# Optimization experiments

Measured on AMD Instinct MI355X. Metric: run time of the kernel, lower is better.

The kernel has to match this reference:

```python
import jax, jax.numpy as jnp
import numpy as np

EPS = 1e-5
DIL = 2
PAD = 2  # dilation * (kernel_size - 1) // 2


def _conv(x, w, dil, pad):
    return jax.lax.conv_general_dilated(
        x, w, window_strides=(1, 1), padding=[(pad, pad), (pad, pad)],
        rhs_dilation=(dil, dil), dimension_numbers=('NCHW', 'OIHW', 'NCHW'))


def _bn(x, g, b):
    # BatchNorm2d in training mode: per-channel batch stats over (N,H,W)
    m = x.mean(axis=(0, 2, 3), keepdims=True)
    v = x.var(axis=(0, 2, 3), keepdims=True)
    return (x - m) * jax.lax.rsqrt(v + EPS) * g[None, :, None, None] + b[None, :, None, None]


def _deform_conv(x, offset, w, dil=DIL, pad=PAD):
    # torchvision deform_conv2d v1 (no modulation): offset [B, 2*K, H, W] with
    # channel ordering (dy_0, dx_0, dy_1, dx_1, ...), kernel tap k = ky*3 + kx.
    B, C, H, W = x.shape
    Co = w.shape[0]
    K = 9
    off = offset.reshape(B, K, 2, H, W)
    dy, dx = off[:, :, 0], off[:, :, 1]              # [B,K,H,W]
    kr = jnp.arange(3)
    kyy = (jnp.repeat(kr, 3) * dil - pad).astype(x.dtype)   # [K]
    kxx = (jnp.tile(kr, 3) * dil - pad).astype(x.dtype)     # [K]
    hg = jnp.arange(H, dtype=x.dtype)
    wg = jnp.arange(W, dtype=x.dtype)
    py = hg[None, None, :, None] + kyy[None, :, None, None] + dy   # [B,K,H,W]
    px = wg[None, None, None, :] + kxx[None, :, None, None] + dx   # [B,K,H,W]
    y0 = jnp.floor(py)
    x0 = jnp.floor(px)
    wy = py - y0   # [B,K,H,W]
    wx = px - x0
    y0i = y0.astype(jnp.int32)
    x0i = x0.astype(jnp.int32)
    x_flat = x.reshape(B, C, H * W)

    def corner(yi, xi):
        valid = ((yi >= 0) & (yi < H) & (xi >= 0) & (xi < W)).astype(x.dtype)  # [B,K,H,W]
        idx = jnp.clip(yi, 0, H - 1) * W + jnp.clip(xi, 0, W - 1)
        v = jax.vmap(lambda xb, ib: xb[:, ib])(x_flat, idx.reshape(B, -1))    # [B,C,K*H*W]
        return v.reshape(B, C, K, H, W) * valid[:, None]

    v00 = corner(y0i, x0i)
    v01 = corner(y0i, x0i + 1)
    v10 = corner(y0i + 1, x0i)
    v11 = corner(y0i + 1, x0i + 1)
    wy_ = wy[:, None]   # [B,1,K,H,W]
    wx_ = wx[:, None]
    sampled = (v00 * (1 - wy_) * (1 - wx_) + v01 * (1 - wy_) * wx_
               + v10 * wy_ * (1 - wx_) + v11 * wy_ * wx_)          # [B,C,K,H,W]
    return jnp.einsum('bckhw,ock->bohw', sampled, w.reshape(Co, C, K))


def setup_inputs() -> dict:
    key = jax.random.key(0)
    ks = jax.random.split(key, 4)
    B, C, H, W = 4, 256, 56, 56
    x = jax.random.normal(ks[0], (B, C, H, W), dtype=jnp.float32)
    w_off = jax.random.normal(ks[1], (18, C, 3, 3), dtype=jnp.float32) * 0.01
    b_off = jnp.zeros((18,), dtype=jnp.float32)
    w1 = jax.random.normal(ks[2], (C, C, 3, 3), dtype=jnp.float32) * (1.0 / np.sqrt(9 * C))
    w2 = jax.random.normal(ks[3], (C, C, 3, 3), dtype=jnp.float32) * (1.0 / np.sqrt(9 * C))
    gamma1 = jnp.ones((C,), dtype=jnp.float32)
    beta1 = jnp.zeros((C,), dtype=jnp.float32)
    gamma2 = jnp.ones((C,), dtype=jnp.float32)
    beta2 = jnp.zeros((C,), dtype=jnp.float32)
    return {'x': x, 'w_off': w_off, 'b_off': b_off, 'w1': w1, 'gamma1': gamma1,
            'beta1': beta1, 'w2': w2, 'gamma2': gamma2, 'beta2': beta2}


def reference(x, w_off, b_off, w1, gamma1, beta1, w2, gamma2, beta2):
    offset = _conv(x, w_off, DIL, PAD) + b_off[None, :, None, None]   # [B,18,H,W]
    out = _deform_conv(x, offset, w1)
    out = jax.nn.relu(_bn(out, gamma1, beta1))
    out = _conv(out, w2, 1, 1)
    out = _bn(out, gamma2, beta2)
    return jax.nn.relu(out + x)
```

## Files before the change

### kernel.cpp

```cpp
#include <hip/hip_runtime.h>

typedef __bf16 bf16;
typedef bf16 bf16x4 __attribute__((ext_vector_type(4)));
typedef bf16 bf16x8 __attribute__((ext_vector_type(8)));
typedef float f32x4 __attribute__((ext_vector_type(4)));

#define CH 256
#define HH 56
#define WW 56
#define HW 3136
#define MM 12544
#define KT 2304

__device__ __forceinline__ void gll16(const bf16* g, bf16* l) {
  __builtin_amdgcn_global_load_lds(
      (const __attribute__((address_space(1))) void*)g,
      (__attribute__((address_space(3))) void*)l, 16, 0, 0);
}

__global__ __launch_bounds__(256) void nchw2nhwc_k(const float* __restrict__ x,
                                                   bf16* __restrict__ o) {
  __shared__ float t[32][33];
  const int b = blockIdx.z, hw0 = blockIdx.x * 32, c0 = blockIdx.y * 32;
  const int tid = threadIdx.x;
  {
    const int cl = tid >> 3, hwl = (tid & 7) * 4;
    f32x4 v = *(const f32x4*)&x[(size_t)(b * CH + c0 + cl) * HW + hw0 + hwl];
#pragma unroll
    for (int i = 0; i < 4; ++i) t[cl][hwl + i] = v[i];
  }
  __syncthreads();
  const int hwl = tid >> 3, cl = (tid & 7) * 4;
  bf16x4 ov;
#pragma unroll
  for (int i = 0; i < 4; ++i) ov[i] = (bf16)t[cl + i][hwl];
  *(bf16x4*)&o[(size_t)(b * HW + hw0 + hwl) * CH + c0 + cl] = ov;
}

__global__ void reorder_w_k(const float* __restrict__ in, bf16* __restrict__ out,
                            int Nsrc, int Ntot) {
  const int idx = blockIdx.x * 256 + threadIdx.x;
  if (idx >= Ntot * KT) return;
  const int o = idx / KT, r = idx - o * KT;
  const int k = r >> 8, c = r & 255;
  float v = (o < Nsrc) ? in[(size_t)(o * CH + c) * 9 + k] : 0.f;
  out[idx] = (bf16)v;
}

__global__ __launch_bounds__(256) void build_deform_k(
    const bf16* __restrict__ xn, const float* __restrict__ offb,
    const float* __restrict__ boff, bf16* __restrict__ A1) {
  const int tid = threadIdx.x;
  const int m = blockIdx.x * 32 + (tid >> 3);
  const int l7 = tid & 7;
  const int b = m / HW, hw = m - b * HW;
  const int h = hw / WW, w = hw - h * WW;
  const float* orow = offb + m * 18;
  const bf16* xb = xn + (size_t)b * HW * CH;
  bf16* dst = A1 + (size_t)m * KT;
  for (int tap = 0; tap < 9; ++tap) {
    const int ky = tap / 3, kx = tap - ky * 3;
    const float dy = orow[2 * tap] + boff[2 * tap];
    const float dx = orow[2 * tap + 1] + boff[2 * tap + 1];
    const float py = (float)(h + ky * 2 - 2) + dy;
    const float px = (float)(w + kx * 2 - 2) + dx;
    const float y0f = floorf(py), x0f = floorf(px);
    const int y0 = (int)y0f, x0 = (int)x0f;
    const float wy = py - y0f, wx = px - x0f;
    const float w00 = (1.f - wy) * (1.f - wx), w01 = (1.f - wy) * wx;
    const float w10 = wy * (1.f - wx), w11 = wy * wx;
    const bool vy0 = (unsigned)y0 < HH, vy1 = (unsigned)(y0 + 1) < HH;
    const bool vx0 = (unsigned)x0 < WW, vx1 = (unsigned)(x0 + 1) < WW;
    const bf16* p00 = xb + (long long)(y0 * WW + x0) * CH;
#pragma unroll
    for (int j = 0; j < 4; ++j) {
      const int cc = j * 64 + l7 * 8;
      bf16x8 v00 = {}, v01 = {}, v10 = {}, v11 = {};
      if (vy0 && vx0) v00 = *(const bf16x8*)(p00 + cc);
      if (vy0 && vx1) v01 = *(const bf16x8*)(p00 + CH + cc);
      if (vy1 && vx0) v10 = *(const bf16x8*)(p00 + WW * CH + cc);
      if (vy1 && vx1) v11 = *(const bf16x8*)(p00 + WW * CH + CH + cc);
      bf16x8 o;
#pragma unroll
      for (int i = 0; i < 8; ++i)
        o[i] = (bf16)(w00 * (float)v00[i] + w01 * (float)v01[i] +
                      w10 * (float)v10[i] + w11 * (float)v11[i]);
      *(bf16x8*)(dst + tap * 256 + cc) = o;
    }
  }
}

template <int MODE, int EPI>
__global__ __launch_bounds__(256, 3) void gemm_k(
    const bf16* __restrict__ Asrc, const bf16* __restrict__ Bt,
    const bf16* __restrict__ zp, bf16* __restrict__ outb,
    float* __restrict__ sS, float* __restrict__ sQ,
    float* __restrict__ offout, const int ksteps, const int dil, const int pad) {
  __shared__ __align__(16) bf16 Ab[2][4096];
  __shared__ __align__(16) bf16 Bb[2][4096];
  const int tid = threadIdx.x;
  const int n0 = blockIdx.x * 64, m0 = blockIdx.y * 64;
  const int kbase = blockIdx.z * ksteps * 64;
  const int lane = tid & 63, wv = tid >> 6;
  const int wrM = wv >> 1, wcN = wv & 1;
  const int fr = lane & 15, kg = lane >> 4;
  const int srow = tid >> 3, cpos = tid & 7;
  const int sxor = (cpos ^ (srow & 7)) * 8;

  int bb[2], hh[2], wwv[2];
  const bf16* aptr[2];
  if (MODE == 1) {
#pragma unroll
    for (int pa = 0; pa < 2; ++pa) {
      const int m = m0 + pa * 32 + srow;
      bb[pa] = m / HW;
      const int hw = m - bb[pa] * HW;
      hh[pa] = hw / WW;
      wwv[pa] = hw - hh[pa] * WW;
    }
  } else {
#pragma unroll
    for (int pa = 0; pa < 2; ++pa)
      aptr[pa] = Asrc + (size_t)(m0 + pa * 32 + srow) * KT + kbase + sxor;
  }
  const bf16* bptr[2];
#pragma unroll
  for (int pb = 0; pb < 2; ++pb)
    bptr[pb] = Bt + (size_t)(n0 + pb * 32 + srow) * KT + kbase + sxor;

  f32x4 acc[2][2] = {};

  auto STAGE = [&](int kt, int buf) {
    const int kk = kbase + kt * 64;
#pragma unroll
    for (int pa = 0; pa < 2; ++pa) {
      const bf16* as;
      if (MODE == 0) {
        as = aptr[pa] + kt * 64;
      } else {
        const int tap = kk >> 8, coff = kk & 255;
        const int ky = tap / 3, kx = tap - ky * 3;
        const int y = hh[pa] + ky * dil - pad, xx = wwv[pa] + kx * dil - pad;
        const bool ok = ((unsigned)y < HH) && ((unsigned)xx < WW);
        as = ok ? Asrc + ((size_t)(bb[pa] * HW + y * WW + xx) * CH + coff + sxor)
                : zp + sxor;
      }
      gll16(as, &Ab[buf][(pa * 32 + srow) * 64 + cpos * 8]);
    }
#pragma unroll
    for (int pb = 0; pb < 2; ++pb)
      gll16(bptr[pb] + kt * 64, &Bb[buf][(pb * 32 + srow) * 64 + cpos * 8]);
  };

  auto COMPUTE = [&](int buf) {
#pragma unroll
    for (int kh = 0; kh < 2; ++kh) {
      bf16x8 af[2], bv[2];
#pragma unroll
      for (int mf = 0; mf < 2; ++mf) {
        const int row = wrM * 32 + mf * 16 + fr;
        const int g = (kh * 4 + kg) ^ (row & 7);
        af[mf] = *(const bf16x8*)&Ab[buf][row * 64 + g * 8];
      }
#pragma unroll
      for (int nf = 0; nf < 2; ++nf) {
        const int row = wcN * 32 + nf * 16 + fr;
        const int g = (kh * 4 + kg) ^ (row & 7);
        bv[nf] = *(const bf16x8*)&Bb[buf][row * 64 + g * 8];
      }
#pragma unroll
      for (int mf = 0; mf < 2; ++mf)
#pragma unroll
        for (int nf = 0; nf < 2; ++nf)
          acc[mf][nf] = __builtin_amdgcn_mfma_f32_16x16x32_bf16(af[mf], bv[nf],
                                                                acc[mf][nf], 0, 0, 0);
    }
  };

  STAGE(0, 0);
  __syncthreads();
  int buf = 0;
  for (int kt = 0; kt < ksteps; ++kt) {
    if (kt + 1 < ksteps) STAGE(kt + 1, buf ^ 1);
    COMPUTE(buf);
    __syncthreads();
    buf ^= 1;
  }

  if (EPI == 1) {
#pragma unroll
    for (int mf = 0; mf < 2; ++mf) {
      const int rr = m0 + wrM * 32 + mf * 16 + kg * 4;
#pragma unroll
      for (int nf = 0; nf < 2; ++nf) {
        const int col = n0 + wcN * 32 + nf * 16 + fr;
#pragma unroll
        for (int r = 0; r < 4; ++r)
          outb[(size_t)(rr + r) * CH + col] = (bf16)acc[mf][nf][r];
      }
    }
    float ps[2], pq[2];
#pragma unroll
    for (int nf = 0; nf < 2; ++nf) {
      float s = 0.f, q = 0.f;
#pragma unroll
      for (int mf = 0; mf < 2; ++mf)
#pragma unroll
        for (int r = 0; r < 4; ++r) {
          const float v = acc[mf][nf][r];
          s += v;
          q += v * v;
        }
      s += __shfl_xor(s, 16);
      s += __shfl_xor(s, 32);
      q += __shfl_xor(q, 16);
      q += __shfl_xor(q, 32);
      ps[nf] = s;
      pq[nf] = q;
    }
    float* red = (float*)&Ab[0][0];
    if (tid < 128) red[tid] = 0.f;
    __syncthreads();
    if (kg == 0) {
#pragma unroll
      for (int nf = 0; nf < 2; ++nf) {
        const int cb = wcN * 32 + nf * 16 + fr;
        atomicAdd(&red[cb], ps[nf]);
        atomicAdd(&red[64 + cb], pq[nf]);
      }
    }
    __syncthreads();
    if (tid < 64) {
      atomicAdd(&sS[n0 + tid], red[tid]);
      atomicAdd(&sQ[n0 + tid], red[64 + tid]);
    }
  } else {
#pragma unroll
    for (int mf = 0; mf < 2; ++mf) {
      const int rr = m0 + wrM * 32 + mf * 16 + kg * 4;
#pragma unroll
      for (int nf = 0; nf < 2; ++nf) {
        const int col = n0 + wcN * 32 + nf * 16 + fr;
        if (col < 18) {
#pragma unroll
          for (int r = 0; r < 4; ++r)
            atomicAdd(&offout[(size_t)(rr + r) * 18 + col], acc[mf][nf][r]);
        }
      }
    }
  }
}

__global__ void affine_k(const float* __restrict__ s, const float* __restrict__ sq,
                         const float* __restrict__ g, const float* __restrict__ be,
                         float* __restrict__ sc, float* __restrict__ bi) {
  const int c = threadIdx.x;
  const float inv = 1.f / (float)MM;
  const float mean = s[c] * inv;
  const float var = sq[c] * inv - mean * mean;
  const float scale = g[c] * rsqrtf(var + 1e-5f);
  sc[c] = scale;
  bi[c] = be[c] - mean * scale;
}

__global__ __launch_bounds__(256) void a1_kb(const bf16* __restrict__ in,
                                             const float* __restrict__ sc,
                                             const float* __restrict__ bi,
                                             bf16* __restrict__ out) {
  const size_t idx = (size_t)(blockIdx.x * 256 + threadIdx.x) * 8;
  const int c0 = (int)(idx & 255);
  bf16x8 v = *(const bf16x8*)&in[idx];
  bf16x8 o;
#pragma unroll
  for (int i = 0; i < 8; ++i) {
    float r = (float)v[i] * sc[c0 + i] + bi[c0 + i];
    o[i] = (bf16)(r > 0.f ? r : 0.f);
  }
  *(bf16x8*)&out[idx] = o;
}

__global__ __launch_bounds__(256) void final_kb(const bf16* __restrict__ o2,
                                                const float* __restrict__ x,
                                                const float* __restrict__ sc,
                                                const float* __restrict__ bi,
                                                float* __restrict__ out) {
  __shared__ float t[32][33];
  const int b = blockIdx.z, hw0 = blockIdx.x * 32, o0 = blockIdx.y * 32;
  const int tid = threadIdx.x;
  {
    const int hwl = tid >> 3, ol = (tid & 7) * 4;
    bf16x4 v = *(const bf16x4*)&o2[(size_t)(b * HW + hw0 + hwl) * CH + o0 + ol];
#pragma unroll
    for (int i = 0; i < 4; ++i) t[ol + i][hwl] = (float)v[i];
  }
  __syncthreads();
  const int ol = tid >> 3, hwl = (tid & 7) * 4;
  const int ch = o0 + ol;
  const float s = sc[ch], bb = bi[ch];
  const size_t xi = (size_t)(b * CH + ch) * HW + hw0 + hwl;
  f32x4 xv = *(const f32x4*)&x[xi];
  f32x4 r;
#pragma unroll
  for (int i = 0; i < 4; ++i) {
    float v = t[ol][hwl + i] * s + bb + xv[i];
    r[i] = v > 0.f ? v : 0.f;
  }
  *(f32x4*)&out[xi] = r;
}

#define WS_XN 0ULL
#define WS_W1T 6422528ULL
#define WS_W2T 7602176ULL
#define WS_WOF 8781824ULL
#define WS_OFFB 9076736ULL
#define WS_A1 9979904ULL
#define WS_O1 67782656ULL
#define WS_ACT 74205184ULL
#define WS_O2 80627712ULL
#define WS_ZP 87050240ULL
#define WS_STAT 87054336ULL
#define WS_SCB 87058432ULL

extern "C" void kernel_launch(void* const* d_in, const int* in_sizes, int n_in,
                              void* d_out, int out_size, void* d_ws, size_t ws_size,
                              hipStream_t stream) {
  const float* x = (const float*)d_in[0];
  const float* w_off = (const float*)d_in[1];
  const float* b_off = (const float*)d_in[2];
  const float* w1 = (const float*)d_in[3];
  const float* g1 = (const float*)d_in[4];
  const float* be1 = (const float*)d_in[5];
  const float* w2 = (const float*)d_in[6];
  const float* g2 = (const float*)d_in[7];
  const float* be2 = (const float*)d_in[8];
  float* out = (float*)d_out;
  char* ws = (char*)d_ws;

  bf16* xn = (bf16*)(ws + WS_XN);
  bf16* w1t = (bf16*)(ws + WS_W1T);
  bf16* w2t = (bf16*)(ws + WS_W2T);
  bf16* wof = (bf16*)(ws + WS_WOF);
  float* offb = (float*)(ws + WS_OFFB);
  bf16* A1 = (bf16*)(ws + WS_A1);
  bf16* o1 = (bf16*)(ws + WS_O1);
  bf16* act = (bf16*)(ws + WS_ACT);
  bf16* o2 = (bf16*)(ws + WS_O2);
  bf16* zp = (bf16*)(ws + WS_ZP);
  float* s1 = (float*)(ws + WS_STAT);
  float* sq1 = (float*)(ws + WS_STAT + 1024);
  float* s2 = (float*)(ws + WS_STAT + 2048);
  float* sq2 = (float*)(ws + WS_STAT + 3072);
  float* sc1 = (float*)(ws + WS_SCB);
  float* bi1 = (float*)(ws + WS_SCB + 1024);
  float* sc2 = (float*)(ws + WS_SCB + 2048);
  float* bi2 = (float*)(ws + WS_SCB + 3072);

  hipMemsetAsync(ws + WS_ZP, 0, 8192, stream);
  hipMemsetAsync(ws + WS_OFFB, 0, 903168, stream);

  nchw2nhwc_k<<<dim3(98, 8, 4), 256, 0, stream>>>(x, xn);
  reorder_w_k<<<2304, 256, 0, stream>>>(w1, w1t, 256, 256);
  reorder_w_k<<<2304, 256, 0, stream>>>(w2, w2t, 256, 256);
  reorder_w_k<<<576, 256, 0, stream>>>(w_off, wof, 18, 64);

  gemm_k<1, 0><<<dim3(1, 196, 4), 256, 0, stream>>>(xn, wof, zp, nullptr, nullptr,
                                                    nullptr, offb, 9, 2, 2);
  build_deform_k<<<392, 256, 0, stream>>>(xn, offb, b_off, A1);

  gemm_k<0, 1><<<dim3(4, 196, 1), 256, 0, stream>>>(A1, w1t, zp, o1, s1, sq1,
                                                    nullptr, 36, 0, 0);
  affine_k<<<1, 256, 0, stream>>>(s1, sq1, g1, be1, sc1, bi1);
  a1_kb<<<1568, 256, 0, stream>>>(o1, sc1, bi1, act);

  gemm_k<1, 1><<<dim3(4, 196, 1), 256, 0, stream>>>(act, w2t, zp, o2, s2, sq2,
                                                    nullptr, 36, 1, 1);
  affine_k<<<1, 256, 0, stream>>>(s2, sq2, g2, be2, sc2, bi2);

  final_kb<<<dim3(98, 8, 4), 256, 0, stream>>>(o2, x, sc2, bi2, out);
}
```

Before: 232.5 us.

## Use 128x128 split-K GEMM tiles with fp32 atomic output and separate stats pass

Replaces the 64x64 double-buffered GEMM for the two main convolutions with a 128x128 tile kernel that splits K three ways and accumulates into an fp32 buffer via atomicAdd. BN statistics move out of the GEMM epilogue into a separate stats kernel, and the downstream activation and final kernels read fp32 instead of bf16. The larger tiles aim for more data reuse per load. In exchange the new kernel is single-buffered, adds buffer memsets and heavy global atomic traffic, and doubles intermediate bytes.

```diff
diff --git a/kernel.cpp b/kernel.cpp
--- a/kernel.cpp
+++ b/kernel.cpp
@@ -90,17 +90,14 @@
   }
 }
 
-template <int MODE, int EPI>
-__global__ __launch_bounds__(256, 3) void gemm_k(
-    const bf16* __restrict__ Asrc, const bf16* __restrict__ Bt,
-    const bf16* __restrict__ zp, bf16* __restrict__ outb,
-    float* __restrict__ sS, float* __restrict__ sQ,
-    float* __restrict__ offout, const int ksteps, const int dil, const int pad) {
+__global__ __launch_bounds__(256, 3) void offset_gemm_k(
+    const bf16* __restrict__ xn, const bf16* __restrict__ wof,
+    const bf16* __restrict__ zp, float* __restrict__ offout) {
   __shared__ __align__(16) bf16 Ab[2][4096];
   __shared__ __align__(16) bf16 Bb[2][4096];
   const int tid = threadIdx.x;
-  const int n0 = blockIdx.x * 64, m0 = blockIdx.y * 64;
-  const int kbase = blockIdx.z * ksteps * 64;
+  const int m0 = blockIdx.y * 64;
+  const int kbase = blockIdx.z * 576;
   const int lane = tid & 63, wv = tid >> 6;
   const int wrM = wv >> 1, wcN = wv & 1;
   const int fr = lane & 15, kg = lane >> 4;
@@ -108,43 +105,32 @@
   const int sxor = (cpos ^ (srow & 7)) * 8;
 
   int bb[2], hh[2], wwv[2];
-  const bf16* aptr[2];
-  if (MODE == 1) {
-#pragma unroll
-    for (int pa = 0; pa < 2; ++pa) {
-      const int m = m0 + pa * 32 + srow;
-      bb[pa] = m / HW;
-      const int hw = m - bb[pa] * HW;
-      hh[pa] = hw / WW;
-      wwv[pa] = hw - hh[pa] * WW;
-    }
-  } else {
-#pragma unroll
-    for (int pa = 0; pa < 2; ++pa)
-      aptr[pa] = Asrc + (size_t)(m0 + pa * 32 + srow) * KT + kbase + sxor;
+#pragma unroll
+  for (int pa = 0; pa < 2; ++pa) {
+    const int m = m0 + pa * 32 + srow;
+    bb[pa] = m / HW;
+    const int hw = m - bb[pa] * HW;
+    hh[pa] = hw / WW;
+    wwv[pa] = hw - hh[pa] * WW;
   }
   const bf16* bptr[2];
 #pragma unroll
   for (int pb = 0; pb < 2; ++pb)
-    bptr[pb] = Bt + (size_t)(n0 + pb * 32 + srow) * KT + kbase + sxor;
+    bptr[pb] = wof + (size_t)(pb * 32 + srow) * KT + kbase + sxor;
 
   f32x4 acc[2][2] = {};
 
   auto STAGE = [&](int kt, int buf) {
     const int kk = kbase + kt * 64;
+    const int tap = kk >> 8, coff = kk & 255;
+    const int ky = tap / 3, kx = tap - ky * 3;
 #pragma unroll
     for (int pa = 0; pa < 2; ++pa) {
-      const bf16* as;
-      if (MODE == 0) {
-        as = aptr[pa] + kt * 64;
-      } else {
-        const int tap = kk >> 8, coff = kk & 255;
-        const int ky = tap / 3, kx = tap - ky * 3;
-        const int y = hh[pa] + ky * dil - pad, xx = wwv[pa] + kx * dil - pad;
-        const bool ok = ((unsigned)y < HH) && ((unsigned)xx < WW);
-        as = ok ? Asrc + ((size_t)(bb[pa] * HW + y * WW + xx) * CH + coff + sxor)
-                : zp + sxor;
-      }
+      const int y = hh[pa] + ky * 2 - 2, xx = wwv[pa] + kx * 2 - 2;
+      const bool ok = ((unsigned)y < HH) && ((unsigned)xx < WW);
+      const bf16* as =
+          ok ? xn + ((size_t)(bb[pa] * HW + y * WW + xx) * CH + coff + sxor)
+             : zp + sxor;
       gll16(as, &Ab[buf][(pa * 32 + srow) * 64 + cpos * 8]);
     }
 #pragma unroll
@@ -180,75 +166,136 @@
   STAGE(0, 0);
   __syncthreads();
   int buf = 0;
-  for (int kt = 0; kt < ksteps; ++kt) {
-    if (kt + 1 < ksteps) STAGE(kt + 1, buf ^ 1);
+  for (int kt = 0; kt < 9; ++kt) {
+    if (kt + 1 < 9) STAGE(kt + 1, buf ^ 1);
     COMPUTE(buf);
     __syncthreads();
     buf ^= 1;
   }
-
-  if (EPI == 1) {
-#pragma unroll
-    for (int mf = 0; mf < 2; ++mf) {
-      const int rr = m0 + wrM * 32 + mf * 16 + kg * 4;
-#pragma unroll
-      for (int nf = 0; nf < 2; ++nf) {
-        const int col = n0 + wcN * 32 + nf * 16 + fr;
+#pragma unroll
+  for (int mf = 0; mf < 2; ++mf) {
+    const int rr = m0 + wrM * 32 + mf * 16 + kg * 4;
+#pragma unroll
+    for (int nf = 0; nf < 2; ++nf) {
+      const int col = wcN * 32 + nf * 16 + fr;
+      if (col < 18) {
 #pragma unroll
         for (int r = 0; r < 4; ++r)
-          outb[(size_t)(rr + r) * CH + col] = (bf16)acc[mf][nf][r];
-      }
-    }
-    float ps[2], pq[2];
-#pragma unroll
-    for (int nf = 0; nf < 2; ++nf) {
-      float s = 0.f, q = 0.f;
-#pragma unroll
-      for (int mf = 0; mf < 2; ++mf)
-#pragma unroll
-        for (int r = 0; r < 4; ++r) {
-          const float v = acc[mf][nf][r];
-          s += v;
-          q += v * v;
-        }
-      s += __shfl_xor(s, 16);
-      s += __shfl_xor(s, 32);
-      q += __shfl_xor(q, 16);
-      q += __shfl_xor(q, 32);
-      ps[nf] = s;
-      pq[nf] = q;
-    }
-    float* red = (float*)&Ab[0][0];
-    if (tid < 128) red[tid] = 0.f;
+          atomicAdd(&offout[(size_t)(rr + r) * 18 + col], acc[mf][nf][r]);
+      }
+    }
+  }
+}
+
+template <int MODE>
+__global__ __launch_bounds__(256) void gemm128_k(
+    const bf16* __restrict__ Asrc, const bf16* __restrict__ Bt,
+    const bf16* __restrict__ zp, float* __restrict__ outp,
+    const int dil, const int pad) {
+  __shared__ __align__(16) bf16 Ab[128 * 64];
+  __shared__ __align__(16) bf16 Bb[128 * 64];
+  const int tid = threadIdx.x;
+  const int n0 = blockIdx.x * 128, m0 = blockIdx.y * 128;
+  const int kbase = blockIdx.z * 768;
+  const int lane = tid & 63, wv = tid >> 6;
+  const int wrM = wv >> 1, wcN = wv & 1;
+  const int fr = lane & 15, kg = lane >> 4;
+  const int srow = tid >> 3, cpos = tid & 7;
+  const int sxor = (cpos ^ (srow & 7)) * 8;
+
+  int bb[4], hh[4], wwv[4];
+  const bf16* aptr[4];
+  if (MODE == 1) {
+#pragma unroll
+    for (int q = 0; q < 4; ++q) {
+      const int m = m0 + q * 32 + srow;
+      bb[q] = m / HW;
+      const int hw = m - bb[q] * HW;
+      hh[q] = hw / WW;
+      wwv[q] = hw - hh[q] * WW;
+    }
+  } else {
+#pragma unroll
+    for (int q = 0; q < 4; ++q)
+      aptr[q] = Asrc + (size_t)(m0 + q * 32 + srow) * KT + kbase + sxor;
+  }
+  const bf16* bptr[4];
+#pragma unroll
+  for (int q = 0; q < 4; ++q)
+    bptr[q] = Bt + (size_t)(n0 + q * 32 + srow) * KT + kbase + sxor;
+
+  f32x4 acc[4][4] = {};
+
+  for (int kt = 0; kt < 12; ++kt) {
+    const int kk = kbase + kt * 64;
+#pragma unroll
+    for (int q = 0; q < 4; ++q) {
+      const bf16* as;
+      if (MODE == 0) {
+        as = aptr[q] + kt * 64;
+      } else {
+        const int tap = kk >> 8, coff = kk & 255;
+        const int ky = tap / 3, kx = tap - ky * 3;
+        const int y = hh[q] + ky * dil - pad, xx = wwv[q] + kx * dil - pad;
+        const bool ok = ((unsigned)y < HH) && ((unsigned)xx < WW);
+        as = ok ? Asrc + ((size_t)(bb[q] * HW + y * WW + xx) * CH + coff + sxor)
+                : zp + sxor;
+      }
+      gll16(as, &Ab[(q * 32 + srow) * 64 + cpos * 8]);
+      gll16(bptr[q] + kt * 64, &Bb[(q * 32 + srow) * 64 + cpos * 8]);
+    }
     __syncthreads();
-    if (kg == 0) {
-#pragma unroll
-      for (int nf = 0; nf < 2; ++nf) {
-        const int cb = wcN * 32 + nf * 16 + fr;
-        atomicAdd(&red[cb], ps[nf]);
-        atomicAdd(&red[64 + cb], pq[nf]);
-      }
+#pragma unroll
+    for (int kh = 0; kh < 2; ++kh) {
+      bf16x8 af[4], bv[4];
+#pragma unroll
+      for (int mf = 0; mf < 4; ++mf) {
+        const int row = wrM * 64 + mf * 16 + fr;
+        const int g = (kh * 4 + kg) ^ (row & 7);
+        af[mf] = *(const bf16x8*)&Ab[row * 64 + g * 8];
+      }
+#pragma unroll
+      for (int nf = 0; nf < 4; ++nf) {
+        const int row = wcN * 64 + nf * 16 + fr;
+        const int g = (kh * 4 + kg) ^ (row & 7);
+        bv[nf] = *(const bf16x8*)&Bb[row * 64 + g * 8];
+      }
+#pragma unroll
+      for (int mf = 0; mf < 4; ++mf)
+#pragma unroll
+        for (int nf = 0; nf < 4; ++nf)
+          acc[mf][nf] = __builtin_amdgcn_mfma_f32_16x16x32_bf16(af[mf], bv[nf],
+                                                                acc[mf][nf], 0, 0, 0);
     }
     __syncthreads();
-    if (tid < 64) {
-      atomicAdd(&sS[n0 + tid], red[tid]);
-      atomicAdd(&sQ[n0 + tid], red[64 + tid]);
-    }
-  } else {
-#pragma unroll
-    for (int mf = 0; mf < 2; ++mf) {
-      const int rr = m0 + wrM * 32 + mf * 16 + kg * 4;
-#pragma unroll
-      for (int nf = 0; nf < 2; ++nf) {
-        const int col = n0 + wcN * 32 + nf * 16 + fr;
-        if (col < 18) {
-#pragma unroll
-          for (int r = 0; r < 4; ++r)
-            atomicAdd(&offout[(size_t)(rr + r) * 18 + col], acc[mf][nf][r]);
-        }
-      }
-    }
-  }
+  }
+
+#pragma unroll
+  for (int mf = 0; mf < 4; ++mf) {
+    const int rr = m0 + wrM * 64 + mf * 16 + kg * 4;
+#pragma unroll
+    for (int nf = 0; nf < 4; ++nf) {
+      const int col = n0 + wcN * 64 + nf * 16 + fr;
+#pragma unroll
+      for (int r = 0; r < 4; ++r)
+        atomicAdd(&outp[(size_t)(rr + r) * CH + col], acc[mf][nf][r]);
+    }
+  }
+}
+
+__global__ __launch_bounds__(256) void stats_f32(const float* __restrict__ d,
+                                                 float* __restrict__ s,
+                                                 float* __restrict__ sq) {
+  const int c = threadIdx.x;
+  const int m0 = blockIdx.x * 64;
+  float a = 0.f, q = 0.f;
+  for (int i = 0; i < 64; ++i) {
+    float v = d[(size_t)(m0 + i) * CH + c];
+    a += v;
+    q += v * v;
+  }
+  atomicAdd(&s[c], a);
+  atomicAdd(&sq[c], q);
 }
 
 __global__ void affine_k(const float* __restrict__ s, const float* __restrict__ sq,
@@ -263,35 +310,41 @@
   bi[c] = be[c] - mean * scale;
 }
 
-__global__ __launch_bounds__(256) void a1_kb(const bf16* __restrict__ in,
-                                             const float* __restrict__ sc,
-                                             const float* __restrict__ bi,
-                                             bf16* __restrict__ out) {
+__global__ __launch_bounds__(256) void a1_f32(const float* __restrict__ in,
+                                              const float* __restrict__ sc,
+                                              const float* __restrict__ bi,
+                                              bf16* __restrict__ out) {
   const size_t idx = (size_t)(blockIdx.x * 256 + threadIdx.x) * 8;
   const int c0 = (int)(idx & 255);
-  bf16x8 v = *(const bf16x8*)&in[idx];
+  f32x4 v0 = *(const f32x4*)&in[idx];
+  f32x4 v1 = *(const f32x4*)&in[idx + 4];
   bf16x8 o;
 #pragma unroll
-  for (int i = 0; i < 8; ++i) {
-    float r = (float)v[i] * sc[c0 + i] + bi[c0 + i];
+  for (int i = 0; i < 4; ++i) {
+    float r = v0[i] * sc[c0 + i] + bi[c0 + i];
     o[i] = (bf16)(r > 0.f ? r : 0.f);
   }
+#pragma unroll
+  for (int i = 0; i < 4; ++i) {
+    float r = v1[i] * sc[c0 + 4 + i] + bi[c0 + 4 + i];
+    o[4 + i] = (bf16)(r > 0.f ? r : 0.f);
+  }
   *(bf16x8*)&out[idx] = o;
 }
 
-__global__ __launch_bounds__(256) void final_kb(const bf16* __restrict__ o2,
-                                                const float* __restrict__ x,
-                                                const float* __restrict__ sc,
-                                                const float* __restrict__ bi,
-                                                float* __restrict__ out) {
+__global__ __launch_bounds__(256) void final_f32(const float* __restrict__ o2,
+                                                 const float* __restrict__ x,
+                                                 const float* __restrict__ sc,
+                                                 const float* __restrict__ bi,
+                                                 float* __restrict__ out) {
   __shared__ float t[32][33];
   const int b = blockIdx.z, hw0 = blockIdx.x * 32, o0 = blockIdx.y * 32;
   const int tid = threadIdx.x;
   {
     const int hwl = tid >> 3, ol = (tid & 7) * 4;
-    bf16x4 v = *(const bf16x4*)&o2[(size_t)(b * HW + hw0 + hwl) * CH + o0 + ol];
-#pragma unroll
-    for (int i = 0; i < 4; ++i) t[ol + i][hwl] = (float)v[i];
+    f32x4 v = *(const f32x4*)&o2[(size_t)(b * HW + hw0 + hwl) * CH + o0 + ol];
+#pragma unroll
+    for (int i = 0; i < 4; ++i) t[ol + i][hwl] = v[i];
   }
   __syncthreads();
   const int ol = tid >> 3, hwl = (tid & 7) * 4;
@@ -314,9 +367,8 @@
 #define WS_WOF 8781824ULL
 #define WS_OFFB 9076736ULL
 #define WS_A1 9979904ULL
-#define WS_O1 67782656ULL
-#define WS_ACT 74205184ULL
-#define WS_O2 80627712ULL
+#define WS_OBUF 67782656ULL
+#define WS_ACT 80627712ULL
 #define WS_ZP 87050240ULL
 #define WS_STAT 87054336ULL
 #define WS_SCB 87058432ULL
@@ -342,9 +394,8 @@
   bf16* wof = (bf16*)(ws + WS_WOF);
   float* offb = (float*)(ws + WS_OFFB);
   bf16* A1 = (bf16*)(ws + WS_A1);
-  bf16* o1 = (bf16*)(ws + WS_O1);
+  float* obuf = (float*)(ws + WS_OBUF);
   bf16* act = (bf16*)(ws + WS_ACT);
-  bf16* o2 = (bf16*)(ws + WS_O2);
   bf16* zp = (bf16*)(ws + WS_ZP);
   float* s1 = (float*)(ws + WS_STAT);
   float* sq1 = (float*)(ws + WS_STAT + 1024);
@@ -357,24 +408,28 @@
 
   hipMemsetAsync(ws + WS_ZP, 0, 8192, stream);
   hipMemsetAsync(ws + WS_OFFB, 0, 903168, stream);
+  hipMemsetAsync(ws + WS_OBUF, 0, 12845056, stream);
 
   nchw2nhwc_k<<<dim3(98, 8, 4), 256, 0, stream>>>(x, xn);
   reorder_w_k<<<2304, 256, 0, stream>>>(w1, w1t, 256, 256);
   reorder_w_k<<<2304, 256, 0, stream>>>(w2, w2t, 256, 256);
   reorder_w_k<<<576, 256, 0, stream>>>(w_off, wof, 18, 64);
 
-  gemm_k<1, 0><<<dim3(1, 196, 4), 256, 0, stream>>>(xn, wof, zp, nullptr, nullptr,
-                                                    nullptr, offb, 9, 2, 2);
+  offset_gemm_k<<<dim3(1, 196, 4), 256, 0, stream>>>(xn, wof, zp, offb);
+
   build_deform_k<<<392, 256, 0, stream>>>(xn, offb, b_off, A1);
 
-  gemm_k<0, 1><<<dim3(4, 196, 1), 256, 0, stream>>>(A1, w1t, zp, o1, s1, sq1,
-                                                    nullptr, 36, 0, 0);
+  gemm128_k<0><<<dim3(2, 98, 3), 256, 0, stream>>>(A1, w1t, zp, obuf, 0, 0);
+
+  stats_f32<<<196, 256, 0, stream>>>(obuf, s1, sq1);
   affine_k<<<1, 256, 0, stream>>>(s1, sq1, g1, be1, sc1, bi1);
-  a1_kb<<<1568, 256, 0, stream>>>(o1, sc1, bi1, act);
-
-  gemm_k<1, 1><<<dim3(4, 196, 1), 256, 0, stream>>>(act, w2t, zp, o2, s2, sq2,
-                                                    nullptr, 36, 1, 1);
+  a1_f32<<<1568, 256, 0, stream>>>(obuf, sc1, bi1, act);
+
+  hipMemsetAsync(ws + WS_OBUF, 0, 12845056, stream);
+  gemm128_k<1><<<dim3(2, 98, 3), 256, 0, stream>>>(act, w2t, zp, obuf, 1, 1);
+
+  stats_f32<<<196, 256, 0, stream>>>(obuf, s2, sq2);
   affine_k<<<1, 256, 0, stream>>>(s2, sq2, g2, be2, sc2, bi2);
 
-  final_kb<<<dim3(98, 8, 4), 256, 0, stream>>>(o2, x, sc2, bi2, out);
-}
+  final_f32<<<dim3(98, 8, 4), 256, 0, stream>>>(obuf, x, sc2, bi2, out);
+}
```

Result: slower. 285.1 us (+22.6%).

## Deepen GEMM prefetch to two stages with vmcnt waits and swizzle block order

Applied to the files above, without the earlier changes.

The GEMM main loop now issues loads two k-steps ahead into the double buffer. It waits with explicit s_waitcnt vmcnt counts and raw barriers instead of __syncthreads, so the global_load_lds copies overlap more of the MFMA compute. The two 256-channel conv GEMMs also launch on a 1D grid with a remapped block index, so that concurrently running blocks cluster by XCD or tile for better L2 reuse. The hand-written vmcnt(4) depends on how many loads each STAGE issues per thread. It also reuses a buffer right after the barrier, so it risks races if that count is wrong.

```diff
diff --git a/kernel.cpp b/kernel.cpp
--- a/kernel.cpp
+++ b/kernel.cpp
@@ -90,7 +90,7 @@
   }
 }
 
-template <int MODE, int EPI>
+template <int MODE, int EPI, int SWZ>
 __global__ __launch_bounds__(256, 3) void gemm_k(
     const bf16* __restrict__ Asrc, const bf16* __restrict__ Bt,
     const bf16* __restrict__ zp, bf16* __restrict__ outb,
@@ -99,7 +99,16 @@
   __shared__ __align__(16) bf16 Ab[2][4096];
   __shared__ __align__(16) bf16 Bb[2][4096];
   const int tid = threadIdx.x;
-  const int n0 = blockIdx.x * 64, m0 = blockIdx.y * 64;
+  int n0, m0;
+  if (SWZ) {
+    const int gid = blockIdx.x;
+    const int swz = (gid & 7) * 98 + (gid >> 3);
+    n0 = (swz & 3) * 64;
+    m0 = (swz >> 2) * 64;
+  } else {
+    n0 = blockIdx.x * 64;
+    m0 = blockIdx.y * 64;
+  }
   const int kbase = blockIdx.z * ksteps * 64;
   const int lane = tid & 63, wv = tid >> 6;
   const int wrM = wv >> 1, wcN = wv & 1;
@@ -178,12 +187,20 @@
   };
 
   STAGE(0, 0);
-  __syncthreads();
+  STAGE(1, 1);
   int buf = 0;
   for (int kt = 0; kt < ksteps; ++kt) {
-    if (kt + 1 < ksteps) STAGE(kt + 1, buf ^ 1);
+    if (kt + 1 < ksteps) {
+      asm volatile("s_waitcnt vmcnt(4)" ::: "memory");
+    } else {
+      asm volatile("s_waitcnt vmcnt(0)" ::: "memory");
+    }
+    __builtin_amdgcn_s_barrier();
+    __builtin_amdgcn_sched_barrier(0);
     COMPUTE(buf);
-    __syncthreads();
+    __builtin_amdgcn_sched_barrier(0);
+    __builtin_amdgcn_s_barrier();
+    if (kt + 2 < ksteps) STAGE(kt + 2, buf);
     buf ^= 1;
   }
 
@@ -363,17 +380,18 @@
   reorder_w_k<<<2304, 256, 0, stream>>>(w2, w2t, 256, 256);
   reorder_w_k<<<576, 256, 0, stream>>>(w_off, wof, 18, 64);
 
-  gemm_k<1, 0><<<dim3(1, 196, 4), 256, 0, stream>>>(xn, wof, zp, nullptr, nullptr,
-                                                    nullptr, offb, 9, 2, 2);
+  gemm_k<1, 0, 0><<<dim3(1, 196, 4), 256, 0, stream>>>(
+      xn, wof, zp, nullptr, nullptr, nullptr, offb, 9, 2, 2);
+
   build_deform_k<<<392, 256, 0, stream>>>(xn, offb, b_off, A1);
 
-  gemm_k<0, 1><<<dim3(4, 196, 1), 256, 0, stream>>>(A1, w1t, zp, o1, s1, sq1,
-                                                    nullptr, 36, 0, 0);
+  gemm_k<0, 1, 1><<<dim3(784), 256, 0, stream>>>(A1, w1t, zp, o1, s1, sq1,
+                                                 nullptr, 36, 0, 0);
   affine_k<<<1, 256, 0, stream>>>(s1, sq1, g1, be1, sc1, bi1);
   a1_kb<<<1568, 256, 0, stream>>>(o1, sc1, bi1, act);
 
-  gemm_k<1, 1><<<dim3(4, 196, 1), 256, 0, stream>>>(act, w2t, zp, o2, s2, sq2,
-                                                    nullptr, 36, 1, 1);
+  gemm_k<1, 1, 1><<<dim3(784), 256, 0, stream>>>(act, w2t, zp, o2, s2, sq2,
+                                                 nullptr, 36, 1, 1);
   affine_k<<<1, 256, 0, stream>>>(s2, sq2, g2, be2, sc2, bi2);
 
   final_kb<<<dim3(98, 8, 4), 256, 0, stream>>>(o2, x, sc2, bi2, out);
```

Result: faster. 215.9 us (-7.2%).
